# Kernel optimization log

Hardware: AMD Instinct MI355X
Metric: run time of the kernel (lower is better)

The kernel has to match this reference:

```python
import jax, jax.numpy as jnp
import numpy as np

N_NODES = 50000
N_EDGES = 800000
D = 128
BATCHSIZE = 64


def setup_inputs() -> dict:
    key = jax.random.key(0)
    k1, k2, k3, k4 = jax.random.split(key, 4)
    x = jax.random.normal(k1, (N_NODES, D), dtype=jnp.float32)
    eps = jnp.zeros((1,), dtype=jnp.float32)
    W_pred = jax.random.normal(k2, (D, D), dtype=jnp.float32) * (1.0 / np.sqrt(D))
    b_pred = jnp.zeros((D,), dtype=jnp.float32)
    edge_index = jax.random.randint(k3, (2, N_EDGES), 0, N_NODES, dtype=jnp.int64)
    batch = jnp.sort(jax.random.randint(k4, (N_NODES,), 0, BATCHSIZE, dtype=jnp.int64))
    return {"x": x, "eps": eps, "W_pred": W_pred, "b_pred": b_pred,
            "edge_index": edge_index, "batch": batch}


def reference(x, eps, W_pred, b_pred, edge_index, batch):
    src, dst = edge_index[0], edge_index[1]
    # spmm: sum of neighbor features for each destination node [N, D]
    agg = jax.ops.segment_sum(x[src], dst, num_segments=N_NODES)
    # eps-weighted self update (apply_func=None, norm=None)
    out = (1.0 + eps) * x + agg
    out = jax.nn.relu(out)  # activation='relu'
    # linear_prediction then per-graph scatter-add pooling
    pooled = out @ W_pred + b_pred  # [N, pooled_features]
    pooled2 = jax.ops.segment_sum(pooled, batch, num_segments=BATCHSIZE)  # [B, pooled]
    return out, pooled2
```

## Files before the change

### kernel.cpp

```cpp
#include <hip/hip_runtime.h>
#include <hip/hip_bf16.h>

#define N_NODES 50000
#define N_EDGES 800000
#define D 128
#define BATCHSIZE 64

#define CHUNK_BITS 7
#define CHUNK 128
#define NBUCKETS 391
#define NBUCKETS_PAD 392
#define CAP 2400

#define FB_TILE 4096
#define NTILES ((N_EDGES + FB_TILE - 1) / FB_TILE)
#define SLICES 4
#define SLICE_B 98
#define FB_THREADS 256
#define FB_GRID (NTILES * SLICES)

__device__ inline unsigned short f2bf(float f) {
    union { float f; unsigned u; } c; c.f = f;
    unsigned u = c.u;
    return (unsigned short)((u + 0x7fffu + ((u >> 16) & 1u)) >> 16);
}

__device__ inline float4 bf4_to_f4(uint2 u) {
    union { unsigned u; float f; } a, b, c, d;
    a.u = u.x << 16; b.u = u.x & 0xffff0000u;
    c.u = u.y << 16; d.u = u.y & 0xffff0000u;
    float4 r; r.x = a.f; r.y = b.f; r.z = c.f; r.w = d.f;
    return r;
}

__global__ __launch_bounds__(FB_THREADS) void bin_convert_kernel(
    const float* __restrict__ x,
    unsigned short* __restrict__ xb,
    const int* __restrict__ edge_index,
    int* __restrict__ gcur,
    int* __restrict__ bucket,
    float* __restrict__ pooled2)
{
    __shared__ int hist[SLICE_B];
    __shared__ int gbase[SLICE_B];

    int t = threadIdx.x;
    int blk = blockIdx.x;

    for (int i = blk * FB_THREADS + t; i < BATCHSIZE * D; i += FB_GRID * FB_THREADS)
        pooled2[i] = 0.0f;

    if (xb != nullptr) {
        const int TOT4 = N_NODES * D / 4;
        for (int i = blk * FB_THREADS + t; i < TOT4; i += FB_GRID * FB_THREADS) {
            float4 v = *(const float4*)(x + (size_t)i * 4);
            uint2 pk;
            pk.x = (unsigned)f2bf(v.x) | ((unsigned)f2bf(v.y) << 16);
            pk.y = (unsigned)f2bf(v.z) | ((unsigned)f2bf(v.w) << 16);
            *(uint2*)(xb + (size_t)i * 4) = pk;
        }
    }

    int tile = blk >> 2;
    int sl   = blk & 3;
    int blo  = sl * SLICE_B;
    int bhi  = blo + SLICE_B; if (bhi > NBUCKETS) bhi = NBUCKETS;
    int nb   = bhi - blo;

    for (int i = t; i < SLICE_B; i += FB_THREADS) hist[i] = 0;
    __syncthreads();

    int base = tile * FB_TILE;
    int lim = N_EDGES - base; if (lim > FB_TILE) lim = FB_TILE;

    int bkt[16];
    int pack[16];
#pragma unroll
    for (int j = 0; j < 4; ++j) {
        int rel = j * FB_THREADS + t;
        int e4 = rel * 4;
#pragma unroll
        for (int k = 0; k < 4; ++k) bkt[j * 4 + k] = -1;
        if (e4 < lim) {
            int4 s4 = *(const int4*)(edge_index + base + e4);
            int4 d4 = *(const int4*)(edge_index + N_EDGES + base + e4);
            int ss[4] = { s4.x, s4.y, s4.z, s4.w };
            int dd[4] = { d4.x, d4.y, d4.z, d4.w };
#pragma unroll
            for (int k = 0; k < 4; ++k) {
                int b = (dd[k] >> CHUNK_BITS) - blo;
                if ((unsigned)b < (unsigned)nb) {
                    bkt[j * 4 + k] = b;
                    pack[j * 4 + k] = (ss[k] << CHUNK_BITS) | (dd[k] & (CHUNK - 1));
                    atomicAdd(&hist[b], 1);
                }
            }
        }
    }
    __syncthreads();

    for (int i = t; i < nb; i += FB_THREADS) {
        int c = hist[i];
        gbase[i] = c ? atomicAdd(&gcur[blo + i], c) : 0;
        hist[i] = 0;
    }
    __syncthreads();

#pragma unroll
    for (int k = 0; k < 16; ++k) {
        int b = bkt[k];
        if (b >= 0) {
            int pos = gbase[b] + atomicAdd(&hist[b], 1);
            if (pos < CAP) bucket[(size_t)(blo + b) * CAP + pos] = pack[k];
        }
    }
}

template<bool BF16>
__global__ __launch_bounds__(1024) void gather_kernel(
    const float* __restrict__ x,
    const unsigned short* __restrict__ xb,
    const float* __restrict__ eps,
    const int* __restrict__ batch,
    const int* __restrict__ gcur,
    const int* __restrict__ bucket,
    const float* __restrict__ W,
    const float* __restrict__ b_pred,
    float* __restrict__ out,
    float* __restrict__ pooled2)
{
    __shared__ int   ebuf[CAP];
    __shared__ int   sorted[CAP];
    __shared__ int   hist[CHUNK];
    __shared__ int   offs[CHUNK + 1];
    __shared__ int   cursor[CHUNK];
    __shared__ float pool[8 * D];
    __shared__ int   pcount[8];

    int c = blockIdx.x;
    int t = threadIdx.x;
    int lane = t & 31;
    int g = t >> 5;

    if (t < CHUNK) hist[t] = 0;
    if (t < 8) pcount[t] = 0;
    for (int i = t; i < 8 * D; i += 1024) pool[i] = 0.0f;
    int cnt = gcur[c];
    if (cnt > CAP) cnt = CAP;
    __syncthreads();

    for (int i = t; i < cnt; i += 1024) {
        int p = bucket[(size_t)c * CAP + i];
        ebuf[i] = p;
        atomicAdd(&hist[p & (CHUNK - 1)], 1);
    }
    __syncthreads();

    if (t < 64) {
        int h0 = hist[2 * t], h1 = hist[2 * t + 1];
        int tot = h0 + h1;
        int incl = tot;
#pragma unroll
        for (int o = 1; o < 64; o <<= 1) {
            int y = __shfl_up(incl, o, 64);
            if (t >= o) incl += y;
        }
        int excl = incl - tot;
        offs[2 * t] = excl;          cursor[2 * t] = excl;
        offs[2 * t + 1] = excl + h0; cursor[2 * t + 1] = excl + h0;
        if (t == 63) offs[CHUNK] = incl;
    }
    __syncthreads();

    for (int i = t; i < cnt; i += 1024) {
        int p = ebuf[i];
        int pos = atomicAdd(&cursor[p & (CHUNK - 1)], 1);
        sorted[pos] = p >> CHUNK_BITS;
    }
    __syncthreads();

    int node0 = c << CHUNK_BITS;
    int base_b = batch[node0];
    float scale = 1.0f + eps[0];
    int dv_cur = -1;
    float4 ps = make_float4(0.f, 0.f, 0.f, 0.f);

#pragma unroll
    for (int k = 0; k < 4; ++k) {
        int d = 4 * g + k;
        int node = node0 + d;
        if (node >= N_NODES) break;
        int start = offs[d], end = offs[d + 1];
        float4 acc = make_float4(0.f, 0.f, 0.f, 0.f);
        int i = start;
        if (BF16) {
            for (; i + 4 <= end; i += 4) {
                int s0 = sorted[i], s1 = sorted[i + 1];
                int s2 = sorted[i + 2], s3 = sorted[i + 3];
                uint2 u0 = *(const uint2*)(xb + (size_t)s0 * D + lane * 4);
                uint2 u1 = *(const uint2*)(xb + (size_t)s1 * D + lane * 4);
                uint2 u2 = *(const uint2*)(xb + (size_t)s2 * D + lane * 4);
                uint2 u3 = *(const uint2*)(xb + (size_t)s3 * D + lane * 4);
                float4 v0 = bf4_to_f4(u0), v1 = bf4_to_f4(u1);
                float4 v2 = bf4_to_f4(u2), v3 = bf4_to_f4(u3);
                acc.x += (v0.x + v1.x) + (v2.x + v3.x);
                acc.y += (v0.y + v1.y) + (v2.y + v3.y);
                acc.z += (v0.z + v1.z) + (v2.z + v3.z);
                acc.w += (v0.w + v1.w) + (v2.w + v3.w);
            }
            for (; i < end; ++i) {
                uint2 u0 = *(const uint2*)(xb + (size_t)sorted[i] * D + lane * 4);
                float4 v0 = bf4_to_f4(u0);
                acc.x += v0.x; acc.y += v0.y; acc.z += v0.z; acc.w += v0.w;
            }
        } else {
            for (; i + 4 <= end; i += 4) {
                int s0 = sorted[i], s1 = sorted[i + 1];
                int s2 = sorted[i + 2], s3 = sorted[i + 3];
                const float4 v0 = *(const float4*)(x + (size_t)s0 * D + lane * 4);
                const float4 v1 = *(const float4*)(x + (size_t)s1 * D + lane * 4);
                const float4 v2 = *(const float4*)(x + (size_t)s2 * D + lane * 4);
                const float4 v3 = *(const float4*)(x + (size_t)s3 * D + lane * 4);
                acc.x += (v0.x + v1.x) + (v2.x + v3.x);
                acc.y += (v0.y + v1.y) + (v2.y + v3.y);
                acc.z += (v0.z + v1.z) + (v2.z + v3.z);
                acc.w += (v0.w + v1.w) + (v2.w + v3.w);
            }
            for (; i < end; ++i) {
                const float4 v0 = *(const float4*)(x + (size_t)sorted[i] * D + lane * 4);
                acc.x += v0.x; acc.y += v0.y; acc.z += v0.z; acc.w += v0.w;
            }
        }
        const float4 xv = *(const float4*)(x + (size_t)node * D + lane * 4);
        float4 o;
        o.x = fmaxf(fmaf(scale, xv.x, acc.x), 0.0f);
        o.y = fmaxf(fmaf(scale, xv.y, acc.y), 0.0f);
        o.z = fmaxf(fmaf(scale, xv.z, acc.z), 0.0f);
        o.w = fmaxf(fmaf(scale, xv.w, acc.w), 0.0f);
        *(float4*)(out + (size_t)node * D + lane * 4) = o;

        int dv = batch[node] - base_b;
        if (dv < 8) {
            if (dv != dv_cur) {
                if (dv_cur >= 0) {
                    float* pp = &pool[dv_cur * D + lane * 4];
                    atomicAdd(pp + 0, ps.x); atomicAdd(pp + 1, ps.y);
                    atomicAdd(pp + 2, ps.z); atomicAdd(pp + 3, ps.w);
                }
                ps = make_float4(0.f, 0.f, 0.f, 0.f);
                dv_cur = dv;
            }
            ps.x += o.x; ps.y += o.y; ps.z += o.z; ps.w += o.w;
            if (lane == 0) atomicAdd(&pcount[dv], 1);
        }
    }
    if (dv_cur >= 0) {
        float* pp = &pool[dv_cur * D + lane * 4];
        atomicAdd(pp + 0, ps.x); atomicAdd(pp + 1, ps.y);
        atomicAdd(pp + 2, ps.z); atomicAdd(pp + 3, ps.w);
    }
    __syncthreads();

    int lastnode = node0 + CHUNK - 1;
    if (lastnode >= N_NODES) lastnode = N_NODES - 1;
    int used = batch[lastnode] - base_b + 1;
    if (used > 8) used = 8;
    if (t < D) {
        for (int dv = 0; dv < used; ++dv) {
            float acc = (float)pcount[dv] * b_pred[t];
            const float* prow = &pool[dv * D];
#pragma unroll 8
            for (int k = 0; k < D; ++k) {
                acc = fmaf(prow[k], W[(size_t)k * D + t], acc);
            }
            atomicAdd(&pooled2[(size_t)(base_b + dv) * D + t], acc);
        }
    }
}


__global__ void edge_scatter_kernel(const float* __restrict__ x,
                                    const int* __restrict__ edge_index,
                                    float* __restrict__ agg) {
    int tid = blockIdx.x * blockDim.x + threadIdx.x;
    int lane = tid & 31;
    int e = tid >> 5;
    if (e >= N_EDGES) return;
    int src = edge_index[e];
    int dst = edge_index[N_EDGES + e];
    const float4 v = *(const float4*)(x + (size_t)src * D + lane * 4);
    float* dp = agg + (size_t)dst * D + lane * 4;
    atomicAdd(dp + 0, v.x);
    atomicAdd(dp + 1, v.y);
    atomicAdd(dp + 2, v.z);
    atomicAdd(dp + 3, v.w);
}

__global__ void finalize_kernel(const float* __restrict__ x,
                                const float* __restrict__ eps,
                                const int* __restrict__ batch,
                                float* __restrict__ out,
                                float* __restrict__ Sf,
                                float* __restrict__ counts) {
    int tid = blockIdx.x * blockDim.x + threadIdx.x;
    int lane = tid & 31;
    int node = tid >> 5;
    if (node >= N_NODES) return;
    float scale = 1.0f + eps[0];
    const float4 xv = *(const float4*)(x + (size_t)node * D + lane * 4);
    float4 av = *(float4*)(out + (size_t)node * D + lane * 4);
    float4 o;
    o.x = fmaxf(fmaf(scale, xv.x, av.x), 0.0f);
    o.y = fmaxf(fmaf(scale, xv.y, av.y), 0.0f);
    o.z = fmaxf(fmaf(scale, xv.z, av.z), 0.0f);
    o.w = fmaxf(fmaf(scale, xv.w, av.w), 0.0f);
    *(float4*)(out + (size_t)node * D + lane * 4) = o;
    int b = batch[node];
    float* sp = Sf + (size_t)b * D + lane * 4;
    atomicAdd(sp + 0, o.x);
    atomicAdd(sp + 1, o.y);
    atomicAdd(sp + 2, o.z);
    atomicAdd(sp + 3, o.w);
    if (lane == 0) atomicAdd(counts + b, 1.0f);
}

__global__ void pool_gemm_fallback_kernel(const float* __restrict__ Sf,
                                          const float* __restrict__ counts,
                                          const float* __restrict__ W,
                                          const float* __restrict__ b_pred,
                                          float* __restrict__ pooled2) {
    int b = blockIdx.x;
    int j = threadIdx.x;
    float acc = counts[b] * b_pred[j];
    const float* srow = Sf + (size_t)b * D;
#pragma unroll 8
    for (int k = 0; k < D; ++k) {
        acc = fmaf(srow[k], W[(size_t)k * D + j], acc);
    }
    pooled2[(size_t)b * D + j] = acc;
}

extern "C" void kernel_launch(void* const* d_in, const int* in_sizes, int n_in,
                              void* d_out, int out_size, void* d_ws, size_t ws_size,
                              hipStream_t stream) {
    const float* x      = (const float*)d_in[0];
    const float* eps    = (const float*)d_in[1];
    const float* W_pred = (const float*)d_in[2];
    const float* b_pred = (const float*)d_in[3];
    const int*   eidx   = (const int*)d_in[4];
    const int*   batch  = (const int*)d_in[5];

    float* out     = (float*)d_out;
    float* pooled2 = (float*)d_out + (size_t)N_NODES * D;

    const size_t base_ints = (size_t)NBUCKETS_PAD + (size_t)NBUCKETS * CAP;
    const size_t need_mid  = base_ints * 4;
    const size_t need_full = (base_ints + (size_t)N_NODES * D / 2) * 4;

    if (ws_size >= need_mid) {
        int* gcur   = (int*)d_ws;
        int* bucket = (int*)d_ws + NBUCKETS_PAD;
        bool full = (ws_size >= need_full);
        unsigned short* xb = full ? (unsigned short*)((int*)d_ws + base_ints) : nullptr;

        hipMemsetAsync(gcur, 0, (size_t)NBUCKETS_PAD * 4, stream);

        bin_convert_kernel<<<FB_GRID, FB_THREADS, 0, stream>>>(
            x, xb, eidx, gcur, bucket, pooled2);
        if (full) {
            gather_kernel<true><<<NBUCKETS, 1024, 0, stream>>>(
                x, xb, eps, batch, gcur, bucket, W_pred, b_pred, out, pooled2);
        } else {
            gather_kernel<false><<<NBUCKETS, 1024, 0, stream>>>(
                x, (const unsigned short*)nullptr, eps, batch, gcur, bucket,
                W_pred, b_pred, out, pooled2);
        }
    } else {
        float* Sf      = (float*)d_ws;
        float* countsf = (float*)d_ws + BATCHSIZE * D;
        hipMemsetAsync(out, 0, (size_t)N_NODES * D * sizeof(float), stream);
        hipMemsetAsync(d_ws, 0, (BATCHSIZE * D + BATCHSIZE) * sizeof(float), stream);
        {
            long long total = (long long)N_EDGES * 32;
            int blocks = (int)((total + 255) / 256);
            edge_scatter_kernel<<<blocks, 256, 0, stream>>>(x, eidx, out);
        }
        {
            long long total = (long long)N_NODES * 32;
            int blocks = (int)((total + 255) / 256);
            finalize_kernel<<<blocks, 256, 0, stream>>>(x, eps, batch, out, Sf, countsf);
        }
        pool_gemm_fallback_kernel<<<BATCHSIZE, D, 0, stream>>>(Sf, countsf, W_pred, b_pred, pooled2);
    }
}
```

Measured before the change: 152.5 us.

## Split each gather bucket across two 512-thread blocks and unroll bf16 gather by 8

The gather kernel now launches two blocks per 128-node bucket, each with 512 threads handling 64 destination nodes. Each block scans the full bucket twice, filtering entries to its half, which removes the ebuf staging array and halves the LDS histogram. The bf16 neighbour loop is unrolled to 8 loads per iteration for more memory-level parallelism. The aim is more blocks and better occupancy on a grid of only 391 blocks, at the cost of every bucket being read twice and the small W matmul epilogue being done twice per bucket.

```diff
diff --git a/kernel.cpp b/kernel.cpp
--- a/kernel.cpp
+++ b/kernel.cpp
@@ -18,6 +18,10 @@
 #define SLICE_B 98
 #define FB_THREADS 256
 #define FB_GRID (NTILES * SLICES)
+
+#define GCHUNK 64
+#define GT 512
+#define GGRID (NBUCKETS * 2)
 
 __device__ inline unsigned short f2bf(float f) {
     union { float f; unsigned u; } c; c.f = f;
@@ -117,7 +121,7 @@
 }
 
 template<bool BF16>
-__global__ __launch_bounds__(1024) void gather_kernel(
+__global__ __launch_bounds__(GT, 8) void gather_kernel(
     const float* __restrict__ x,
     const unsigned short* __restrict__ xb,
     const float* __restrict__ eps,
@@ -129,84 +133,98 @@
     float* __restrict__ out,
     float* __restrict__ pooled2)
 {
-    __shared__ int   ebuf[CAP];
     __shared__ int   sorted[CAP];
-    __shared__ int   hist[CHUNK];
-    __shared__ int   offs[CHUNK + 1];
-    __shared__ int   cursor[CHUNK];
+    __shared__ int   hist[GCHUNK];
+    __shared__ int   offs[GCHUNK + 1];
+    __shared__ int   cursor[GCHUNK];
     __shared__ float pool[8 * D];
     __shared__ int   pcount[8];
 
-    int c = blockIdx.x;
+    int blk = blockIdx.x;
+    int c = blk >> 1;
+    int h = blk & 1;
     int t = threadIdx.x;
     int lane = t & 31;
     int g = t >> 5;
 
-    if (t < CHUNK) hist[t] = 0;
+    if (t < GCHUNK) hist[t] = 0;
     if (t < 8) pcount[t] = 0;
-    for (int i = t; i < 8 * D; i += 1024) pool[i] = 0.0f;
+    for (int i = t; i < 8 * D; i += GT) pool[i] = 0.0f;
     int cnt = gcur[c];
     if (cnt > CAP) cnt = CAP;
     __syncthreads();
 
-    for (int i = t; i < cnt; i += 1024) {
-        int p = bucket[(size_t)c * CAP + i];
-        ebuf[i] = p;
-        atomicAdd(&hist[p & (CHUNK - 1)], 1);
-    }
-    __syncthreads();
-
-    if (t < 64) {
-        int h0 = hist[2 * t], h1 = hist[2 * t + 1];
-        int tot = h0 + h1;
+    const int hbase = h << 6;
+    const int* brow = bucket + (size_t)c * CAP;
+
+    for (int i = t; i < cnt; i += GT) {
+        int p = brow[i];
+        int dloc = (p & (CHUNK - 1)) - hbase;
+        if ((unsigned)dloc < (unsigned)GCHUNK) atomicAdd(&hist[dloc], 1);
+    }
+    __syncthreads();
+
+    if (t < GCHUNK) {
+        int tot = hist[t];
         int incl = tot;
 #pragma unroll
         for (int o = 1; o < 64; o <<= 1) {
             int y = __shfl_up(incl, o, 64);
             if (t >= o) incl += y;
         }
-        int excl = incl - tot;
-        offs[2 * t] = excl;          cursor[2 * t] = excl;
-        offs[2 * t + 1] = excl + h0; cursor[2 * t + 1] = excl + h0;
-        if (t == 63) offs[CHUNK] = incl;
-    }
-    __syncthreads();
-
-    for (int i = t; i < cnt; i += 1024) {
-        int p = ebuf[i];
-        int pos = atomicAdd(&cursor[p & (CHUNK - 1)], 1);
-        sorted[pos] = p >> CHUNK_BITS;
-    }
-    __syncthreads();
-
-    int node0 = c << CHUNK_BITS;
-    int base_b = batch[node0];
+        offs[t] = incl - tot;
+        cursor[t] = incl - tot;
+        if (t == GCHUNK - 1) offs[GCHUNK] = incl;
+    }
+    __syncthreads();
+
+    for (int i = t; i < cnt; i += GT) {
+        int p = brow[i];
+        int dloc = (p & (CHUNK - 1)) - hbase;
+        if ((unsigned)dloc < (unsigned)GCHUNK) {
+            int pos = atomicAdd(&cursor[dloc], 1);
+            sorted[pos] = p >> CHUNK_BITS;
+        }
+    }
+    __syncthreads();
+
+    int node0 = (c << CHUNK_BITS) + hbase;
+    int bnode = node0 < N_NODES ? node0 : N_NODES - 1;
+    int base_b = batch[bnode];
     float scale = 1.0f + eps[0];
     int dv_cur = -1;
     float4 ps = make_float4(0.f, 0.f, 0.f, 0.f);
 
 #pragma unroll
     for (int k = 0; k < 4; ++k) {
-        int d = 4 * g + k;
-        int node = node0 + d;
+        int dloc = 4 * g + k;
+        int node = node0 + dloc;
         if (node >= N_NODES) break;
-        int start = offs[d], end = offs[d + 1];
+        int start = offs[dloc], end = offs[dloc + 1];
         float4 acc = make_float4(0.f, 0.f, 0.f, 0.f);
         int i = start;
         if (BF16) {
-            for (; i + 4 <= end; i += 4) {
-                int s0 = sorted[i], s1 = sorted[i + 1];
+            for (; i + 8 <= end; i += 8) {
+                int s0 = sorted[i],     s1 = sorted[i + 1];
                 int s2 = sorted[i + 2], s3 = sorted[i + 3];
+                int s4 = sorted[i + 4], s5 = sorted[i + 5];
+                int s6 = sorted[i + 6], s7 = sorted[i + 7];
                 uint2 u0 = *(const uint2*)(xb + (size_t)s0 * D + lane * 4);
                 uint2 u1 = *(const uint2*)(xb + (size_t)s1 * D + lane * 4);
                 uint2 u2 = *(const uint2*)(xb + (size_t)s2 * D + lane * 4);
                 uint2 u3 = *(const uint2*)(xb + (size_t)s3 * D + lane * 4);
+                uint2 u4 = *(const uint2*)(xb + (size_t)s4 * D + lane * 4);
+                uint2 u5 = *(const uint2*)(xb + (size_t)s5 * D + lane * 4);
+                uint2 u6 = *(const uint2*)(xb + (size_t)s6 * D + lane * 4);
+                uint2 u7 = *(const uint2*)(xb + (size_t)s7 * D + lane * 4);
                 float4 v0 = bf4_to_f4(u0), v1 = bf4_to_f4(u1);
                 float4 v2 = bf4_to_f4(u2), v3 = bf4_to_f4(u3);
-                acc.x += (v0.x + v1.x) + (v2.x + v3.x);
-                acc.y += (v0.y + v1.y) + (v2.y + v3.y);
-                acc.z += (v0.z + v1.z) + (v2.z + v3.z);
-                acc.w += (v0.w + v1.w) + (v2.w + v3.w);
+                float4 v4 = bf4_to_f4(u4), v5 = bf4_to_f4(u5);
+                float4 v6 = bf4_to_f4(u6), v7 = bf4_to_f4(u7);
+                acc.x += ((v0.x + v1.x) + (v2.x + v3.x)) + ((v4.x + v5.x) + (v6.x + v7.x));
+                acc.y += ((v0.y + v1.y) + (v2.y + v3.y)) + ((v4.y + v5.y) + (v6.y + v7.y));
+                acc.z += ((v0.z + v1.z) + (v2.z + v3.z)) + ((v4.z + v5.z) + (v6.z + v7.z));
+                acc.w += ((v0.w + v1.w) + (v2.w + v3.w)) + ((v4.w + v5.w) + (v6.w + v7.w));
             }
             for (; i < end; ++i) {
                 uint2 u0 = *(const uint2*)(xb + (size_t)sorted[i] * D + lane * 4);
@@ -261,10 +279,11 @@
     }
     __syncthreads();
 
-    int lastnode = node0 + CHUNK - 1;
+    int lastnode = node0 + GCHUNK - 1;
     if (lastnode >= N_NODES) lastnode = N_NODES - 1;
     int used = batch[lastnode] - base_b + 1;
     if (used > 8) used = 8;
+    if (used < 0) used = 0;
     if (t < D) {
         for (int dv = 0; dv < used; ++dv) {
             float acc = (float)pcount[dv] * b_pred[t];
@@ -368,10 +387,10 @@
         bin_convert_kernel<<<FB_GRID, FB_THREADS, 0, stream>>>(
             x, xb, eidx, gcur, bucket, pooled2);
         if (full) {
-            gather_kernel<true><<<NBUCKETS, 1024, 0, stream>>>(
+            gather_kernel<true><<<GGRID, GT, 0, stream>>>(
                 x, xb, eps, batch, gcur, bucket, W_pred, b_pred, out, pooled2);
         } else {
-            gather_kernel<false><<<NBUCKETS, 1024, 0, stream>>>(
+            gather_kernel<false><<<GGRID, GT, 0, stream>>>(
                 x, (const unsigned short*)nullptr, eps, batch, gcur, bucket,
                 W_pred, b_pred, out, pooled2);
         }
```

Measured after the change: 155.3 us. Within noise of the previous version (+1.8%).

## Bin edges across all buckets per tile and pad global bucket counters

Applied to the files above, without the earlier changes.

The binning kernel drops the four-way bucket slicing, so each block reads its edge tile once and histograms all buckets in shared memory. The tile shrinks to 2048 edges to keep the block count up. The per-bucket global cursors are padded to a 16-int stride to cut atomic contention and false sharing, and the bf16 conversion now handles 8 floats per thread. In exchange it uses a larger shared histogram, does more global atomics per block, and adds a small extra padded workspace requirement.

```diff
diff --git a/kernel.cpp b/kernel.cpp
--- a/kernel.cpp
+++ b/kernel.cpp
@@ -11,18 +11,18 @@
 #define NBUCKETS 391
 #define NBUCKETS_PAD 392
 #define CAP 2400
-
-#define FB_TILE 4096
+#define GS_PAD 16
+
+#define FB_TILE 2048
 #define NTILES ((N_EDGES + FB_TILE - 1) / FB_TILE)
-#define SLICES 4
-#define SLICE_B 98
 #define FB_THREADS 256
-#define FB_GRID (NTILES * SLICES)
-
-__device__ inline unsigned short f2bf(float f) {
+#define FB_GRID NTILES
+#define EPT 8
+
+__device__ inline unsigned f2bf(float f) {
     union { float f; unsigned u; } c; c.f = f;
     unsigned u = c.u;
-    return (unsigned short)((u + 0x7fffu + ((u >> 16) & 1u)) >> 16);
+    return (u + 0x7fffu + ((u >> 16) & 1u)) >> 16;
 }
 
 __device__ inline float4 bf4_to_f4(uint2 u) {
@@ -39,10 +39,11 @@
     const int* __restrict__ edge_index,
     int* __restrict__ gcur,
     int* __restrict__ bucket,
-    float* __restrict__ pooled2)
+    float* __restrict__ pooled2,
+    int gs)
 {
-    __shared__ int hist[SLICE_B];
-    __shared__ int gbase[SLICE_B];
+    __shared__ int hist[NBUCKETS_PAD];
+    __shared__ int gbase[NBUCKETS_PAD];
 
     int t = threadIdx.x;
     int blk = blockIdx.x;
@@ -51,34 +52,30 @@
         pooled2[i] = 0.0f;
 
     if (xb != nullptr) {
-        const int TOT4 = N_NODES * D / 4;
-        for (int i = blk * FB_THREADS + t; i < TOT4; i += FB_GRID * FB_THREADS) {
-            float4 v = *(const float4*)(x + (size_t)i * 4);
-            uint2 pk;
-            pk.x = (unsigned)f2bf(v.x) | ((unsigned)f2bf(v.y) << 16);
-            pk.y = (unsigned)f2bf(v.z) | ((unsigned)f2bf(v.w) << 16);
-            *(uint2*)(xb + (size_t)i * 4) = pk;
-        }
-    }
-
-    int tile = blk >> 2;
-    int sl   = blk & 3;
-    int blo  = sl * SLICE_B;
-    int bhi  = blo + SLICE_B; if (bhi > NBUCKETS) bhi = NBUCKETS;
-    int nb   = bhi - blo;
-
-    for (int i = t; i < SLICE_B; i += FB_THREADS) hist[i] = 0;
-    __syncthreads();
-
-    int base = tile * FB_TILE;
+        const int TOT8 = N_NODES * D / 8;
+        for (int i = blk * FB_THREADS + t; i < TOT8; i += FB_GRID * FB_THREADS) {
+            float4 v0 = *(const float4*)(x + (size_t)i * 8);
+            float4 v1 = *(const float4*)(x + (size_t)i * 8 + 4);
+            uint4 pk;
+            pk.x = f2bf(v0.x) | (f2bf(v0.y) << 16);
+            pk.y = f2bf(v0.z) | (f2bf(v0.w) << 16);
+            pk.z = f2bf(v1.x) | (f2bf(v1.y) << 16);
+            pk.w = f2bf(v1.z) | (f2bf(v1.w) << 16);
+            *(uint4*)(xb + (size_t)i * 8) = pk;
+        }
+    }
+
+    for (int i = t; i < NBUCKETS_PAD; i += FB_THREADS) hist[i] = 0;
+    __syncthreads();
+
+    int base = blk * FB_TILE;
     int lim = N_EDGES - base; if (lim > FB_TILE) lim = FB_TILE;
 
-    int bkt[16];
-    int pack[16];
-#pragma unroll
-    for (int j = 0; j < 4; ++j) {
-        int rel = j * FB_THREADS + t;
-        int e4 = rel * 4;
+    int bkt[EPT];
+    int pack[EPT];
+#pragma unroll
+    for (int j = 0; j < EPT / 4; ++j) {
+        int e4 = (j * FB_THREADS + t) * 4;
 #pragma unroll
         for (int k = 0; k < 4; ++k) bkt[j * 4 + k] = -1;
         if (e4 < lim) {
@@ -88,30 +85,28 @@
             int dd[4] = { d4.x, d4.y, d4.z, d4.w };
 #pragma unroll
             for (int k = 0; k < 4; ++k) {
-                int b = (dd[k] >> CHUNK_BITS) - blo;
-                if ((unsigned)b < (unsigned)nb) {
-                    bkt[j * 4 + k] = b;
-                    pack[j * 4 + k] = (ss[k] << CHUNK_BITS) | (dd[k] & (CHUNK - 1));
-                    atomicAdd(&hist[b], 1);
-                }
-            }
-        }
-    }
-    __syncthreads();
-
-    for (int i = t; i < nb; i += FB_THREADS) {
+                int b = dd[k] >> CHUNK_BITS;
+                bkt[j * 4 + k] = b;
+                pack[j * 4 + k] = (ss[k] << CHUNK_BITS) | (dd[k] & (CHUNK - 1));
+                atomicAdd(&hist[b], 1);
+            }
+        }
+    }
+    __syncthreads();
+
+    for (int i = t; i < NBUCKETS; i += FB_THREADS) {
         int c = hist[i];
-        gbase[i] = c ? atomicAdd(&gcur[blo + i], c) : 0;
+        gbase[i] = c ? atomicAdd(&gcur[i * gs], c) : 0;
         hist[i] = 0;
     }
     __syncthreads();
 
 #pragma unroll
-    for (int k = 0; k < 16; ++k) {
+    for (int k = 0; k < EPT; ++k) {
         int b = bkt[k];
         if (b >= 0) {
             int pos = gbase[b] + atomicAdd(&hist[b], 1);
-            if (pos < CAP) bucket[(size_t)(blo + b) * CAP + pos] = pack[k];
+            if (pos < CAP) bucket[(size_t)b * CAP + pos] = pack[k];
         }
     }
 }
@@ -127,7 +122,8 @@
     const float* __restrict__ W,
     const float* __restrict__ b_pred,
     float* __restrict__ out,
-    float* __restrict__ pooled2)
+    float* __restrict__ pooled2,
+    int gs)
 {
     __shared__ int   ebuf[CAP];
     __shared__ int   sorted[CAP];
@@ -145,7 +141,7 @@
     if (t < CHUNK) hist[t] = 0;
     if (t < 8) pcount[t] = 0;
     for (int i = t; i < 8 * D; i += 1024) pool[i] = 0.0f;
-    int cnt = gcur[c];
+    int cnt = gcur[(size_t)c * gs];
     if (cnt > CAP) cnt = CAP;
     __syncthreads();
 
@@ -353,27 +349,35 @@
     float* out     = (float*)d_out;
     float* pooled2 = (float*)d_out + (size_t)N_NODES * D;
 
-    const size_t base_ints = (size_t)NBUCKETS_PAD + (size_t)NBUCKETS * CAP;
-    const size_t need_mid  = base_ints * 4;
-    const size_t need_full = (base_ints + (size_t)N_NODES * D / 2) * 4;
+    const size_t xb_ints = (size_t)N_NODES * D / 2;
+    const size_t buck    = (size_t)NBUCKETS * CAP;
+
+    const size_t need_pad_full  = ((size_t)NBUCKETS_PAD * GS_PAD + buck + xb_ints) * 4;
+    const size_t need_full      = ((size_t)NBUCKETS_PAD + buck + xb_ints) * 4;
+    const size_t need_pad_mid   = ((size_t)NBUCKETS_PAD * GS_PAD + buck) * 4;
+    const size_t need_mid       = ((size_t)NBUCKETS_PAD + buck) * 4;
 
     if (ws_size >= need_mid) {
+        int gs = (ws_size >= (ws_size >= need_full ? need_pad_full : need_pad_mid))
+                     ? GS_PAD : 1;
+        size_t gcur_ints = (size_t)NBUCKETS_PAD * gs;
         int* gcur   = (int*)d_ws;
-        int* bucket = (int*)d_ws + NBUCKETS_PAD;
-        bool full = (ws_size >= need_full);
-        unsigned short* xb = full ? (unsigned short*)((int*)d_ws + base_ints) : nullptr;
-
-        hipMemsetAsync(gcur, 0, (size_t)NBUCKETS_PAD * 4, stream);
+        int* bucket = (int*)d_ws + gcur_ints;
+        bool full = (ws_size >= (gs == GS_PAD ? need_pad_full : need_full));
+        unsigned short* xb = full
+            ? (unsigned short*)((int*)d_ws + gcur_ints + buck) : nullptr;
+
+        hipMemsetAsync(gcur, 0, gcur_ints * 4, stream);
 
         bin_convert_kernel<<<FB_GRID, FB_THREADS, 0, stream>>>(
-            x, xb, eidx, gcur, bucket, pooled2);
+            x, xb, eidx, gcur, bucket, pooled2, gs);
         if (full) {
             gather_kernel<true><<<NBUCKETS, 1024, 0, stream>>>(
-                x, xb, eps, batch, gcur, bucket, W_pred, b_pred, out, pooled2);
+                x, xb, eps, batch, gcur, bucket, W_pred, b_pred, out, pooled2, gs);
         } else {
             gather_kernel<false><<<NBUCKETS, 1024, 0, stream>>>(
                 x, (const unsigned short*)nullptr, eps, batch, gcur, bucket,
-                W_pred, b_pred, out, pooled2);
+                W_pred, b_pred, out, pooled2, gs);
         }
     } else {
         float* Sf      = (float*)d_ws;
```

After: 145.8 us. -4.4%, faster.
